# Kernel optimization log

Measured on AMD Instinct MI355X. Metric: run time of the kernel, lower is better.

## Reference

```python
import jax, jax.numpy as jnp
import numpy as np

B, N, HW, PS, FHW = 16, 4096, 224, 8, 56

def _gelu(x):
    return jax.nn.gelu(x, approximate=True)  # tanh approximation, matches nn.GELU(approximate='tanh')

def _conv(x, w, b, stride):
    y = jax.lax.conv_general_dilated(x, w, (stride, stride), [(1, 1), (1, 1)],
                                     dimension_numbers=('NCHW', 'OIHW', 'NCHW'))
    return y + b[None, :, None, None]

def _embed(points):
    # for i in 0..11: append sin(2^i * p) then cos(2^i * p) -> [B,N,48]
    factors = 2.0 ** jnp.arange(12, dtype=points.dtype)
    scaled = points[..., None, :] * factors[:, None]          # [B,N,12,2]
    feats = jnp.concatenate([jnp.sin(scaled), jnp.cos(scaled)], axis=-1)  # [B,N,12,4]
    return feats.reshape(points.shape[0], points.shape[1], 48)

def _extract_patches(fmap, points):
    # fmap [B,C,H,W]; points in [0,1]; bilinear grid_sample, zeros padding, align_corners=True
    Bq, C, H, W = fmap.shape
    centers = points * 2.0 - 1.0
    step = 2.0 / (W - 1)
    half = (PS - 1) / 2.0
    offs = jnp.linspace(-half, half, PS, dtype=fmap.dtype) * step
    offx2d, offy2d = jnp.meshgrid(offs, offs, indexing='ij')   # [ps,ps]
    gx = centers[..., 0][..., None, None] + offx2d             # [B,N,ps,ps]
    gy = centers[..., 1][..., None, None] + offy2d
    # align_corners=True pixel coords
    ix = (gx + 1.0) * 0.5 * (W - 1)
    iy = (gy + 1.0) * 0.5 * (H - 1)
    x0f = jnp.floor(ix); y0f = jnp.floor(iy)
    x0 = x0f.astype(jnp.int32); y0 = y0f.astype(jnp.int32)
    x1 = x0 + 1; y1 = y0 + 1
    wx1 = ix - x0f; wx0 = 1.0 - wx1
    wy1 = iy - y0f; wy0 = 1.0 - wy1
    fflat = fmap.reshape(Bq, C, H * W)

    def corner(xi, yi, w):
        valid = ((xi >= 0) & (xi < W) & (yi >= 0) & (yi < H)).astype(fmap.dtype)
        idx = jnp.clip(yi, 0, H - 1) * W + jnp.clip(xi, 0, W - 1)   # [B,N,ps,ps]
        vals = jax.vmap(lambda f, i: f[:, i])(fflat, idx)           # [B,C,N,ps,ps]
        return vals * (w * valid)[:, None]

    out = (corner(x0, y0, wx0 * wy0) + corner(x1, y0, wx1 * wy0)
           + corner(x0, y1, wx0 * wy1) + corner(x1, y1, wx1 * wy1))  # [B,C,N,ps,ps]
    return out.transpose(0, 2, 1, 3, 4)                              # [B,N,C,ps,ps]

def setup_inputs():
    key = jax.random.key(0)
    ks = jax.random.split(key, 26)
    def w(k, shape):
        fan_in = int(np.prod(shape[1:]))
        return jax.random.normal(k, shape, jnp.float32) * (1.0 / np.sqrt(fan_in))
    inp = {
        'points': jax.random.uniform(ks[0], (B, N, 2), jnp.float32),
        'images': jax.random.normal(ks[1], (B, 3, HW, HW), jnp.float32),
        # plane encoder
        'pw1': w(ks[2], (16, 3, 3, 3)),  'pb1': jnp.zeros((16,), jnp.float32),
        'pw2': w(ks[3], (32, 16, 3, 3)), 'pb2': jnp.zeros((32,), jnp.float32),
        'pw3': w(ks[4], (4, 32, 3, 3)),  'pb3': jnp.zeros((4,), jnp.float32),
        # global encoder
        'gw1': w(ks[5], (4, 3, 3, 3)),   'gb1': jnp.zeros((4,), jnp.float32),
        'gw2': w(ks[6], (8, 4, 3, 3)),   'gb2': jnp.zeros((8,), jnp.float32),
        'gw3': w(ks[7], (16, 8, 3, 3)),  'gb3': jnp.zeros((16,), jnp.float32),
        'gw4': w(ks[8], (32, 16, 3, 3)), 'gb4': jnp.zeros((32,), jnp.float32),
        'gw5': w(ks[9], (64, 32, 3, 3)), 'gb5': jnp.zeros((64,), jnp.float32),
        # point encoder (torch Linear: [out,in])
        'lw1': w(ks[10], (256, 48)),  'lb1': jnp.zeros((256,), jnp.float32),
        'lw2': w(ks[11], (256, 256)), 'lb2': jnp.zeros((256,), jnp.float32),
        # head
        'hw1': w(ks[12], (512, 576)), 'hb1': jnp.zeros((512,), jnp.float32),
        'hw2': w(ks[13], (1, 512)),   'hb2': jnp.zeros((1,), jnp.float32),
    }
    return inp

def reference(points, images, pw1, pb1, pw2, pb2, pw3, pb3,
              gw1, gb1, gw2, gb2, gw3, gb3, gw4, gb4, gw5, gb5,
              lw1, lb1, lw2, lb2, hw1, hb1, hw2, hb2):
    # point branch
    pe = _embed(points)                                         # [B,N,48]
    pf = _gelu(pe @ lw1.T + lb1) @ lw2.T + lb2                  # [B,N,256]
    # plane encoder -> 4x56x56 fmap
    f = _gelu(_conv(images, pw1, pb1, 2))
    f = _gelu(_conv(f, pw2, pb2, 2))
    fmap = _gelu(_conv(f, pw3, pb3, 1))                         # [B,4,56,56]
    # global encoder -> [B,64]
    g = images
    for wg, bg in ((gw1, gb1), (gw2, gb2), (gw3, gb3), (gw4, gb4), (gw5, gb5)):
        g = _gelu(_conv(g, wg, bg, 2))
    gc = g.mean(axis=(2, 3))                                    # AvgPool2d(7)+Flatten -> [B,64]
    gc = jnp.broadcast_to(gc[:, None, :], (points.shape[0], points.shape[1], 64))
    # per-point bilinear patch gather
    patches = _extract_patches(fmap, points).reshape(points.shape[0], points.shape[1], -1)  # [B,N,256]
    fused = jnp.concatenate([pf, patches, gc], axis=-1)         # [B,N,576]
    logit = _gelu(fused @ hw1.T + hb1) @ hw2.T + hb2            # [B,N,1]
    return logit
```

## Files before the change

kernel.cpp:

```cpp
#include <hip/hip_runtime.h>
#include <math.h>

#define BB 16
#define NN 4096
#define M_TOT (BB*NN)
#define TBK 32
#define HBK 64

typedef __attribute__((ext_vector_type(8))) short s8v;
typedef __attribute__((ext_vector_type(4))) float f4v;

__device__ __forceinline__ float gelu_t(float x){
    float u = 1.5957691216057308f * x * (1.0f + 0.044715f*x*x);
    return x / (1.0f + __expf(-u));
}

__device__ __forceinline__ unsigned short f2bf(float f){
    unsigned int u = __float_as_uint(f);
    u += 0x7fffu + ((u >> 16) & 1u);
    return (unsigned short)(u >> 16);
}

#define GLL(src, dst) __builtin_amdgcn_global_load_lds( \
    (const __attribute__((address_space(1))) void*)(src), \
    (__attribute__((address_space(3))) void*)(dst), 16, 0, 0)

template<int CIN, int COUT, int STRIDE, int CHUNK>
__device__ __forceinline__ void conv_dev2(
    const float* __restrict__ in, const float* __restrict__ w,
    const float* __restrict__ bias, float* __restrict__ out,
    int Hin, int Win, int Hout, int Wout, int bx, int by, int b, float* tile)
{
    constexpr int IW = 15*STRIDE + 3;
    constexpr int IH = IW;
    constexpr int PITCH = IW + 1;
    int tid = threadIdx.x;
    int tx = tid & 15, ty = tid >> 4;
    int wo = bx*16 + tx;
    int ho = by*16 + ty;
    int win0 = bx*16*STRIDE - 1;
    int hin0 = by*16*STRIDE - 1;
    bool valid = (wo < Wout) && (ho < Hout);

    float acc[COUT];
    #pragma unroll
    for (int co = 0; co < COUT; ++co) acc[co] = bias[co];

    const float* ib = in + (size_t)(b*CIN)*Hin*Win;
    for (int ci0 = 0; ci0 < CIN; ci0 += CHUNK) {
        __syncthreads();
        for (int idx = tid; idx < CHUNK*IH*IW; idx += 256) {
            int c = idx / (IH*IW), rem = idx - c*(IH*IW);
            int r = rem / IW, cc = rem - r*IW;
            int hi = hin0 + r, wi = win0 + cc;
            float v = 0.f;
            if ((unsigned)hi < (unsigned)Hin && (unsigned)wi < (unsigned)Win)
                v = ib[(size_t)(ci0 + c)*Hin*Win + hi*Win + wi];
            tile[c*IH*PITCH + r*PITCH + cc] = v;
        }
        __syncthreads();
        for (int ci = 0; ci < CHUNK; ++ci) {
            float vv[9];
            const float* tb = tile + ci*IH*PITCH;
            #pragma unroll
            for (int kh = 0; kh < 3; ++kh)
                #pragma unroll
                for (int kw = 0; kw < 3; ++kw)
                    vv[kh*3+kw] = tb[(ty*STRIDE + kh)*PITCH + tx*STRIDE + kw];
            const float* wc = w + (ci0 + ci)*9;
            #pragma unroll
            for (int co = 0; co < COUT; ++co) {
                const float* wp = wc + co*CIN*9;
                #pragma unroll
                for (int k = 0; k < 9; ++k)
                    acc[co] = fmaf(vv[k], wp[k], acc[co]);
            }
        }
    }
    if (valid) {
        size_t obase = ((size_t)b*COUT)*Hout*Wout + (size_t)ho*Wout + wo;
        #pragma unroll
        for (int co = 0; co < COUT; ++co)
            out[obase + (size_t)co*Hout*Wout] = gelu_t(acc[co]);
    }
}

__global__ __launch_bounds__(256) void conv_dual_k(
    const float* __restrict__ in,
    const float* __restrict__ wA, const float* __restrict__ bA,
    const float* __restrict__ wB, const float* __restrict__ bB,
    float* __restrict__ outA, float* __restrict__ outB)
{
    __shared__ float tile[3*33*34];
    const int Hin = 224, Win = 224, Hout = 112, Wout = 112;
    int tid = threadIdx.x;
    int tx = tid & 15, ty = tid >> 4;
    int b = blockIdx.z;
    int wo = blockIdx.x*16 + tx;
    int ho = blockIdx.y*16 + ty;
    int win0 = blockIdx.x*32 - 1;
    int hin0 = blockIdx.y*32 - 1;

    const float* ib = in + (size_t)(b*3)*Hin*Win;
    for (int idx = tid; idx < 3*1089; idx += 256) {
        int c = idx / 1089, rem = idx - c*1089;
        int r = rem / 33, cc = rem - r*33;
        int hi = hin0 + r, wi = win0 + cc;
        float v = 0.f;
        if ((unsigned)hi < (unsigned)Hin && (unsigned)wi < (unsigned)Win)
            v = ib[(size_t)c*Hin*Win + hi*Win + wi];
        tile[c*33*34 + r*34 + cc] = v;
    }
    __syncthreads();

    float accA[16], accB[4];
    #pragma unroll
    for (int co = 0; co < 16; ++co) accA[co] = bA[co];
    #pragma unroll
    for (int co = 0; co < 4; ++co) accB[co] = bB[co];

    #pragma unroll
    for (int ci = 0; ci < 3; ++ci) {
        float vv[9];
        const float* tb = tile + ci*33*34;
        #pragma unroll
        for (int kh = 0; kh < 3; ++kh)
            #pragma unroll
            for (int kw = 0; kw < 3; ++kw)
                vv[kh*3+kw] = tb[(ty*2 + kh)*34 + tx*2 + kw];
        #pragma unroll
        for (int co = 0; co < 16; ++co) {
            const float* wp = wA + co*27 + ci*9;
            #pragma unroll
            for (int k = 0; k < 9; ++k) accA[co] = fmaf(vv[k], wp[k], accA[co]);
        }
        #pragma unroll
        for (int co = 0; co < 4; ++co) {
            const float* wp = wB + co*27 + ci*9;
            #pragma unroll
            for (int k = 0; k < 9; ++k) accB[co] = fmaf(vv[k], wp[k], accB[co]);
        }
    }
    size_t px = (size_t)ho*Wout + wo;
    #pragma unroll
    for (int co = 0; co < 16; ++co)
        outA[((size_t)(b*16 + co))*Hout*Wout + px] = gelu_t(accA[co]);
    #pragma unroll
    for (int co = 0; co < 4; ++co)
        outB[((size_t)(b*4 + co))*Hout*Wout + px] = gelu_t(accB[co]);
}

__global__ __launch_bounds__(256) void conv_pg2_k(
    const float* __restrict__ f1, const float* __restrict__ pw2, const float* __restrict__ pb2, float* __restrict__ f2,
    const float* __restrict__ g1, const float* __restrict__ gw2, const float* __restrict__ gb2, float* __restrict__ g2)
{
    __shared__ float tile[8*33*34];
    int z = blockIdx.z;
    if (z < 32) {
        int b = z >> 1, half = z & 1;
        conv_dev2<16,16,2,8>(f1 + (size_t)b*16*12544, pw2 + half*2304, pb2 + half*16,
                             f2 + ((size_t)(b*32 + half*16))*3136,
                             112,112, 56,56, blockIdx.x, blockIdx.y, 0, tile);
    } else {
        conv_dev2<4,8,2,4>(g1, gw2, gb2, g2, 112,112, 56,56, blockIdx.x, blockIdx.y, z-32, tile);
    }
}

__global__ __launch_bounds__(256) void conv_pg3_k(
    const float* __restrict__ f2, const float* __restrict__ pw3, const float* __restrict__ pb3, float4* __restrict__ fmap4,
    const float* __restrict__ g2, const float* __restrict__ gw3, const float* __restrict__ gb3, float* __restrict__ g3)
{
    __shared__ float tile[8*33*34];
    int z = blockIdx.z;
    if (z < 16) {
        int b = z;
        int idx = blockIdx.x*256 + threadIdx.x;
        if (idx >= 3136) return;
        int ho = idx / 56, wo = idx - ho*56;
        const float* ib = f2 + (size_t)b*32*3136;
        float acc[4];
        #pragma unroll
        for (int co = 0; co < 4; ++co) acc[co] = pb3[co];
        for (int ci = 0; ci < 32; ++ci) {
            const float* ic = ib + (size_t)ci*3136;
            #pragma unroll
            for (int kh = 0; kh < 3; ++kh) {
                int hi = ho - 1 + kh;
                if ((unsigned)hi >= 56u) continue;
                #pragma unroll
                for (int kw = 0; kw < 3; ++kw) {
                    int wi = wo - 1 + kw;
                    if ((unsigned)wi >= 56u) continue;
                    float v = ic[hi*56 + wi];
                    int wofs = ci*9 + kh*3 + kw;
                    #pragma unroll
                    for (int co = 0; co < 4; ++co)
                        acc[co] = fmaf(v, pw3[co*288 + wofs], acc[co]);
                }
            }
        }
        float4 o;
        o.x = gelu_t(acc[0]); o.y = gelu_t(acc[1]);
        o.z = gelu_t(acc[2]); o.w = gelu_t(acc[3]);
        fmap4[(size_t)b*3136 + idx] = o;
    } else {
        if (blockIdx.x >= 4) return;
        int bx = blockIdx.x & 1, by = blockIdx.x >> 1;
        conv_dev2<8,16,2,8>(g2, gw3, gb3, g3, 56,56, 28,28, bx, by, z-16, tile);
    }
}

__global__ __launch_bounds__(256) void g4_k(
    const float* __restrict__ g3, const float* __restrict__ w4,
    const float* __restrict__ b4, float* __restrict__ g4o)
{
    int idx = blockIdx.x*256 + threadIdx.x;
    int co = idx & 31;
    int t = idx >> 5;
    int b = t / 196, px = t - b*196;
    int ho = px / 14, wo = px - ho*14;
    const float* src = g3 + (size_t)b*16*784;
    const float* wp = w4 + co*144;
    float acc = b4[co];
    for (int ci = 0; ci < 16; ++ci) {
        #pragma unroll
        for (int kh = 0; kh < 3; ++kh) {
            int hi = ho*2 - 1 + kh;
            if ((unsigned)hi >= 28u) continue;
            #pragma unroll
            for (int kw = 0; kw < 3; ++kw) {
                int wi = wo*2 - 1 + kw;
                if ((unsigned)wi >= 28u) continue;
                acc = fmaf(src[ci*784 + hi*28 + wi], wp[ci*9 + kh*3 + kw], acc);
            }
        }
    }
    g4o[(size_t)b*6272 + px*32 + co] = gelu_t(acc);
}

__global__ __launch_bounds__(256) void g5_k(
    const float* __restrict__ g4o, const float* __restrict__ w5,
    const float* __restrict__ b5, float* __restrict__ gc)
{
    int idx = blockIdx.x*256 + threadIdx.x;
    int co = idx & 63;
    int t = idx >> 6;
    int b = t / 49, px = t - b*49;
    int ho = px / 7, wo = px - ho*7;
    const float* src = g4o + (size_t)b*6272;
    const float* wp = w5 + co*288;
    float acc = b5[co];
    for (int ci = 0; ci < 32; ++ci) {
        #pragma unroll
        for (int kh = 0; kh < 3; ++kh) {
            int hi = ho*2 - 1 + kh;
            if ((unsigned)hi >= 14u) continue;
            #pragma unroll
            for (int kw = 0; kw < 3; ++kw) {
                int wi = wo*2 - 1 + kw;
                if ((unsigned)wi >= 14u) continue;
                acc = fmaf(src[(hi*14 + wi)*32 + ci], wp[ci*9 + kh*3 + kw], acc);
            }
        }
    }
    atomicAdd(&gc[b*64 + co], gelu_t(acc) * (1.0f/49.0f));
}

__global__ __launch_bounds__(256) void hgc_k(
    const float* __restrict__ gc, const float* __restrict__ hw1,
    const float* __restrict__ hb1, float* __restrict__ hgc)
{
    int idx = blockIdx.x*256 + threadIdx.x;
    int b = idx >> 9, n = idx & 511;
    const float* g = gc + b*64;
    const float* w = hw1 + (size_t)n*576 + 512;
    float s = hb1[n];
    #pragma unroll
    for (int c = 0; c < 64; ++c) s = fmaf(g[c], w[c], s);
    hgc[idx] = s;
}

__global__ void cvtall_k(const float* __restrict__ lw1, const float* __restrict__ lw2,
                         const float* __restrict__ hw1, unsigned short* __restrict__ blw1,
                         unsigned short* __restrict__ blw2, unsigned short* __restrict__ bhw1,
                         float* __restrict__ out, const float* __restrict__ b2,
                         float* __restrict__ gc){
    int i = blockIdx.x*blockDim.x + threadIdx.x;
    if (i < M_TOT) out[i] = b2[0];
    if (i < 1024) gc[i] = 0.f;
    if (i < 256*64) {
        int r = i >> 6, c = i & 63;
        blw1[i] = (c < 48) ? f2bf(lw1[r*48 + c]) : 0;
        return;
    }
    int j = i - 256*64;
    if (j < 256*256) { blw2[j] = f2bf(lw2[j]); return; }
    j -= 256*256;
    if (j < 512*576) bhw1[j] = f2bf(hw1[j]);
}

__global__ __launch_bounds__(512) void mlp12_k(
    const float* __restrict__ points,
    const unsigned short* __restrict__ W1, const float* __restrict__ b1,
    const unsigned short* __restrict__ W2, const float* __restrict__ b2,
    unsigned short* __restrict__ C,
    const float4* __restrict__ fmap4)
{
    __shared__ unsigned short Hd[128*256];
    int tid = threadIdx.x;
    int wv = tid >> 6, lane = tid & 63;
    int q = lane >> 4, lr = lane & 15;
    int mi = wv >> 2, ni = wv & 3;
    size_t m0 = (size_t)blockIdx.x * 128;

    f4v acc1[4][4];
    #pragma unroll
    for (int i = 0; i < 4; ++i)
        #pragma unroll
        for (int j = 0; j < 4; ++j) acc1[i][j] = (f4v){0.f,0.f,0.f,0.f};

    #pragma unroll
    for (int kb = 0; kb < 2; ++kb) {
        int seg = kb*4 + q;
        s8v a[4], b[4];
        #pragma unroll
        for (int t = 0; t < 4; ++t) {
            size_t m = m0 + mi*64 + t*16 + lr;
            float px = points[m*2], py = points[m*2+1];
            union { s8v v; unsigned short u[8]; } pk;
            #pragma unroll
            for (int j = 0; j < 8; ++j) {
                int k = seg*8 + j;
                unsigned short val = 0;
                if (k < 48) {
                    int i2 = k >> 2, rr = k & 3;
                    float f = (float)(1 << i2);
                    float p = (rr & 1) ? py : px;
                    float s = f * p;
                    val = f2bf((rr < 2) ? __sinf(s) : __cosf(s));
                }
                pk.u[j] = val;
            }
            a[t] = pk.v;
        }
        #pragma unroll
        for (int t = 0; t < 4; ++t) {
            int n = ni*64 + t*16 + lr;
            b[t] = *(const s8v*)(W1 + n*64 + seg*8);
        }
        #pragma unroll
        for (int mt = 0; mt < 4; ++mt)
            #pragma unroll
            for (int nt = 0; nt < 4; ++nt)
                acc1[mt][nt] = __builtin_amdgcn_mfma_f32_16x16x32_bf16(a[mt], b[nt], acc1[mt][nt], 0, 0, 0);
    }
    {
        float b1v[4];
        #pragma unroll
        for (int nt = 0; nt < 4; ++nt) b1v[nt] = b1[ni*64 + nt*16 + lr];
        #pragma unroll
        for (int mt = 0; mt < 4; ++mt)
            #pragma unroll
            for (int r4 = 0; r4 < 4; ++r4) {
                int row = mi*64 + mt*16 + q*4 + r4;
                #pragma unroll
                for (int nt = 0; nt < 4; ++nt) {
                    int col = ni*64 + nt*16 + lr;
                    float v = gelu_t(acc1[mt][nt][r4] + b1v[nt]);
                    int p = (col >> 3) ^ (row & 7);
                    Hd[(row*32 + p)*8 + (col & 7)] = f2bf(v);
                }
            }
    }
    __syncthreads();

    f4v acc2[4][4];
    #pragma unroll
    for (int i = 0; i < 4; ++i)
        #pragma unroll
        for (int j = 0; j < 4; ++j) acc2[i][j] = (f4v){0.f,0.f,0.f,0.f};

    #pragma unroll 2
    for (int kt = 0; kt < 8; ++kt) {
        s8v a[4], b[4];
        #pragma unroll
        for (int t = 0; t < 4; ++t) {
            int n = ni*64 + t*16 + lr;
            b[t] = *(const s8v*)(W2 + (size_t)n*256 + kt*32 + q*8);
        }
        #pragma unroll
        for (int t = 0; t < 4; ++t) {
            int row = mi*64 + t*16 + lr;
            int p = (kt*4 + q) ^ (row & 7);
            a[t] = *(const s8v*)(Hd + (row*32 + p)*8);
        }
        #pragma unroll
        for (int mt = 0; mt < 4; ++mt)
            #pragma unroll
            for (int nt = 0; nt < 4; ++nt)
                acc2[mt][nt] = __builtin_amdgcn_mfma_f32_16x16x32_bf16(a[mt], b[nt], acc2[mt][nt], 0, 0, 0);
    }
    {
        float b2v[4];
        #pragma unroll
        for (int nt = 0; nt < 4; ++nt) b2v[nt] = b2[ni*64 + nt*16 + lr];
        #pragma unroll
        for (int mt = 0; mt < 4; ++mt)
            #pragma unroll
            for (int r4 = 0; r4 < 4; ++r4) {
                size_t m = m0 + mi*64 + mt*16 + q*4 + r4;
                #pragma unroll
                for (int nt = 0; nt < 4; ++nt) {
                    int n = ni*64 + nt*16 + lr;
                    C[m*512 + n] = f2bf(acc2[mt][nt][r4] + b2v[nt]);
                }
            }
    }
    #pragma unroll 2
    for (int it = 0; it < 16; ++it) {
        int task = it*512 + tid;
        int ml = task >> 6, ij = task & 63;
        size_t m = m0 + ml;
        int i = ij >> 3, j = ij & 7;
        int b = (int)(m >> 12);
        float px = points[m*2], py = points[m*2+1];
        float cx = px*2.f - 1.f, cy = py*2.f - 1.f;
        const float step = 2.0f/55.0f;
        float gx = cx + ((float)i - 3.5f)*step;
        float gy = cy + ((float)j - 3.5f)*step;
        float ix = (gx + 1.f)*0.5f*55.f;
        float iy = (gy + 1.f)*0.5f*55.f;
        float x0f = floorf(ix), y0f = floorf(iy);
        int x0 = (int)x0f, y0 = (int)y0f;
        int x1 = x0 + 1,  y1 = y0 + 1;
        float wx1 = ix - x0f, wx0 = 1.f - wx1;
        float wy1 = iy - y0f, wy0 = 1.f - wy1;
        float v00 = ((x0>=0)&&(x0<56)&&(y0>=0)&&(y0<56)) ? 1.f : 0.f;
        float v10 = ((x1>=0)&&(x1<56)&&(y0>=0)&&(y0<56)) ? 1.f : 0.f;
        float v01 = ((x0>=0)&&(x0<56)&&(y1>=0)&&(y1<56)) ? 1.f : 0.f;
        float v11 = ((x1>=0)&&(x1<56)&&(y1>=0)&&(y1<56)) ? 1.f : 0.f;
        float w00 = wx0*wy0*v00, w10 = wx1*wy0*v10, w01 = wx0*wy1*v01, w11 = wx1*wy1*v11;
        int cx0 = min(max(x0,0),55), cx1 = min(max(x1,0),55);
        int cy0 = min(max(y0,0),55), cy1 = min(max(y1,0),55);
        const float4* fb = fmap4 + (size_t)b*3136;
        float4 f00 = fb[cy0*56 + cx0], f10 = fb[cy0*56 + cx1];
        float4 f01 = fb[cy1*56 + cx0], f11 = fb[cy1*56 + cx1];
        float4 v;
        v.x = w00*f00.x + w10*f10.x + w01*f01.x + w11*f11.x;
        v.y = w00*f00.y + w10*f10.y + w01*f01.y + w11*f11.y;
        v.z = w00*f00.z + w10*f10.z + w01*f01.z + w11*f11.z;
        v.w = w00*f00.w + w10*f10.w + w01*f01.w + w11*f11.w;
        C[m*512 + 256 +   0 + ij] = f2bf(v.x);
        C[m*512 + 256 +  64 + ij] = f2bf(v.y);
        C[m*512 + 256 + 128 + ij] = f2bf(v.z);
        C[m*512 + 256 + 192 + ij] = f2bf(v.w);
    }
}

__global__ __launch_bounds__(256, 3) void gemm_hd_k(
    const unsigned short* __restrict__ A,
    const unsigned short* __restrict__ W,
    const float* __restrict__ hgc, const float* __restrict__ w2,
    float* __restrict__ out)
{
    __shared__ unsigned short As[64*HBK];
    __shared__ unsigned short Bs[256*HBK];
    __shared__ float red[4*64];
    int tid = threadIdx.x;
    int wv = tid >> 6, lane = tid & 63;
    int q = lane >> 4, lr = lane & 15;
    int nq = wv * 64;
    size_t m0 = (size_t)blockIdx.x * 64;
    int nbase = blockIdx.y * 256;
    int bimg = (int)(m0 >> 12);

    const unsigned short* srcA[2]; unsigned short* dstA[2];
    #pragma unroll
    for (int r = 0; r < 2; ++r) {
        int f = r*256 + tid;
        int row = f >> 3, sl = (f & 7) ^ (row & 7);
        srcA[r] = A + (m0 + row)*512 + sl*8;
        dstA[r] = As + f*8;
    }
    const unsigned short* srcB[8]; unsigned short* dstB[8];
    #pragma unroll
    for (int r = 0; r < 8; ++r) {
        int f = r*256 + tid;
        int row = f >> 3, sl = (f & 7) ^ (row & 7);
        srcB[r] = W + (size_t)(nbase + row)*576 + sl*8;
        dstB[r] = Bs + f*8;
    }

    f4v acc[4][4];
    #pragma unroll
    for (int i = 0; i < 4; ++i)
        #pragma unroll
        for (int j = 0; j < 4; ++j) acc[i][j] = (f4v){0.f,0.f,0.f,0.f};

    for (int k0 = 0; k0 < 512; k0 += HBK) {
        #pragma unroll
        for (int r = 0; r < 2; ++r) { GLL(srcA[r], dstA[r]); srcA[r] += HBK; }
        #pragma unroll
        for (int r = 0; r < 8; ++r) { GLL(srcB[r], dstB[r]); srcB[r] += HBK; }
        __syncthreads();
        #pragma unroll
        for (int kk = 0; kk < 2; ++kk) {
            s8v a[4], b[4];
            #pragma unroll
            for (int t = 0; t < 4; ++t) {
                int row = t*16 + lr;
                int ph = (kk*4 + q) ^ (row & 7);
                a[t] = *(const s8v*)(As + (row*8 + ph)*8);
            }
            #pragma unroll
            for (int t = 0; t < 4; ++t) {
                int row = nq + t*16 + lr;
                int ph = (kk*4 + q) ^ (row & 7);
                b[t] = *(const s8v*)(Bs + (row*8 + ph)*8);
            }
            #pragma unroll
            for (int mt = 0; mt < 4; ++mt)
                #pragma unroll
                for (int nt = 0; nt < 4; ++nt)
                    acc[mt][nt] = __builtin_amdgcn_mfma_f32_16x16x32_bf16(a[mt], b[nt], acc[mt][nt], 0, 0, 0);
        }
        __syncthreads();
    }
    float bv[4], w2v[4];
    #pragma unroll
    for (int nt = 0; nt < 4; ++nt) {
        int n = nbase + nq + nt*16 + lr;
        bv[nt] = hgc[bimg*512 + n];
        w2v[nt] = w2[n];
    }
    #pragma unroll
    for (int mt = 0; mt < 4; ++mt)
        #pragma unroll
        for (int r4 = 0; r4 < 4; ++r4) {
            int ml = mt*16 + q*4 + r4;
            float s = 0.f;
            #pragma unroll
            for (int nt = 0; nt < 4; ++nt)
                s += gelu_t(acc[mt][nt][r4] + bv[nt]) * w2v[nt];
            #pragma unroll
            for (int off = 8; off > 0; off >>= 1) s += __shfl_down(s, off, 16);
            if (lr == 0) red[wv*64 + ml] = s;
        }
    __syncthreads();
    if (tid < 64) {
        float t = red[tid] + red[64 + tid] + red[128 + tid] + red[192 + tid];
        atomicAdd(&out[m0 + tid], t);
    }
}

extern "C" void kernel_launch(void* const* d_in, const int* in_sizes, int n_in,
                              void* d_out, int out_size, void* d_ws, size_t ws_size,
                              hipStream_t stream) {
    const float* points = (const float*)d_in[0];
    const float* images = (const float*)d_in[1];
    const float* pw1 = (const float*)d_in[2];  const float* pb1 = (const float*)d_in[3];
    const float* pw2 = (const float*)d_in[4];  const float* pb2 = (const float*)d_in[5];
    const float* pw3 = (const float*)d_in[6];  const float* pb3 = (const float*)d_in[7];
    const float* gw1 = (const float*)d_in[8];  const float* gb1 = (const float*)d_in[9];
    const float* gw2 = (const float*)d_in[10]; const float* gb2 = (const float*)d_in[11];
    const float* gw3 = (const float*)d_in[12]; const float* gb3 = (const float*)d_in[13];
    const float* gw4 = (const float*)d_in[14]; const float* gb4 = (const float*)d_in[15];
    const float* gw5 = (const float*)d_in[16]; const float* gb5 = (const float*)d_in[17];
    const float* lw1 = (const float*)d_in[18]; const float* lb1 = (const float*)d_in[19];
    const float* lw2 = (const float*)d_in[20]; const float* lb2 = (const float*)d_in[21];
    const float* hw1 = (const float*)d_in[22]; const float* hb1 = (const float*)d_in[23];
    const float* hw2 = (const float*)d_in[24]; const float* hb2 = (const float*)d_in[25];
    float* out = (float*)d_out;

    char* base = (char*)d_ws;
    unsigned short* fused_b = (unsigned short*)base;
    float4* fmap4 = (float4*)(fused_b + (size_t)M_TOT*512);
    float* gc   = (float*)(fmap4 + (size_t)16*3136);
    float* hgc  = gc + 1024;
    unsigned short* blw1 = (unsigned short*)(hgc + 16*512);
    unsigned short* blw2 = blw1 + 256*64;
    unsigned short* bhw1 = blw2 + 256*256;
    float* ct = (float*)base;
    float* f1 = ct;
    float* f2 = f1 + (size_t)16*16*112*112;
    float* g1 = f2 + (size_t)16*32*56*56;
    float* g2 = g1 + (size_t)16*4*112*112;
    float* g3 = g2 + (size_t)16*8*56*56;
    float* g4 = g3 + (size_t)16*16*28*28;

    cvtall_k<<<1472, 256, 0, stream>>>(lw1, lw2, hw1, blw1, blw2, bhw1, out, hb2, gc);
    conv_dual_k<<<dim3(7,7,16), 256, 0, stream>>>(images, pw1, pb1, gw1, gb1, f1, g1);
    conv_pg2_k<<<dim3(4,4,48), 256, 0, stream>>>(f1, pw2, pb2, f2, g1, gw2, gb2, g2);
    conv_pg3_k<<<dim3(13,1,32), 256, 0, stream>>>(f2, pw3, pb3, fmap4, g2, gw3, gb3, g3);
    g4_k<<<392, 256, 0, stream>>>(g3, gw4, gb4, g4);
    g5_k<<<196, 256, 0, stream>>>(g4, gw5, gb5, gc);
    hgc_k<<<32, 256, 0, stream>>>(gc, hw1, hb1, hgc);
    mlp12_k<<<M_TOT/128, 512, 0, stream>>>(points, blw1, lb1, blw2, lb2, fused_b, fmap4);
    gemm_hd_k<<<dim3(M_TOT/64, 2), 256, 0, stream>>>(fused_b, bhw1, hgc, hw2, out);
}
```

Baseline: 427.7 us.

## Move patch gather into g4 kernel, stage positional embedding in LDS, permute hw1 columns

The bilinear patch gather leaves the point-MLP kernel and runs as extra blocks of the small g4 conv launch, so the tiny conv4 work shares one launch with the gather. The gather now writes four channels at a time as one ushort4 store, and the matching hw1 columns are permuted during bf16 conversion so the head GEMM still sees the right order. The MLP kernel computes the sin/cos embedding once per element into swizzled LDS instead of redundantly per wave. g3 and g4o move out of the aliased conv scratch region, because that region overlaps the fused buffer that the gather now writes before the convs' outputs are consumed.

```diff
diff --git a/kernel.cpp b/kernel.cpp
--- a/kernel.cpp
+++ b/kernel.cpp
@@ -4,7 +4,6 @@
 #define BB 16
 #define NN 4096
 #define M_TOT (BB*NN)
-#define TBK 32
 #define HBK 64
 
 typedef __attribute__((ext_vector_type(8))) short s8v;
@@ -210,217 +209,41 @@
     }
 }
 
-__global__ __launch_bounds__(256) void g4_k(
+__global__ __launch_bounds__(256) void k4_k(
     const float* __restrict__ g3, const float* __restrict__ w4,
-    const float* __restrict__ b4, float* __restrict__ g4o)
-{
-    int idx = blockIdx.x*256 + threadIdx.x;
-    int co = idx & 31;
-    int t = idx >> 5;
-    int b = t / 196, px = t - b*196;
-    int ho = px / 14, wo = px - ho*14;
-    const float* src = g3 + (size_t)b*16*784;
-    const float* wp = w4 + co*144;
-    float acc = b4[co];
-    for (int ci = 0; ci < 16; ++ci) {
-        #pragma unroll
-        for (int kh = 0; kh < 3; ++kh) {
-            int hi = ho*2 - 1 + kh;
-            if ((unsigned)hi >= 28u) continue;
-            #pragma unroll
-            for (int kw = 0; kw < 3; ++kw) {
-                int wi = wo*2 - 1 + kw;
-                if ((unsigned)wi >= 28u) continue;
-                acc = fmaf(src[ci*784 + hi*28 + wi], wp[ci*9 + kh*3 + kw], acc);
-            }
-        }
-    }
-    g4o[(size_t)b*6272 + px*32 + co] = gelu_t(acc);
-}
-
-__global__ __launch_bounds__(256) void g5_k(
-    const float* __restrict__ g4o, const float* __restrict__ w5,
-    const float* __restrict__ b5, float* __restrict__ gc)
-{
-    int idx = blockIdx.x*256 + threadIdx.x;
-    int co = idx & 63;
-    int t = idx >> 6;
-    int b = t / 49, px = t - b*49;
-    int ho = px / 7, wo = px - ho*7;
-    const float* src = g4o + (size_t)b*6272;
-    const float* wp = w5 + co*288;
-    float acc = b5[co];
-    for (int ci = 0; ci < 32; ++ci) {
-        #pragma unroll
-        for (int kh = 0; kh < 3; ++kh) {
-            int hi = ho*2 - 1 + kh;
-            if ((unsigned)hi >= 14u) continue;
-            #pragma unroll
-            for (int kw = 0; kw < 3; ++kw) {
-                int wi = wo*2 - 1 + kw;
-                if ((unsigned)wi >= 14u) continue;
-                acc = fmaf(src[(hi*14 + wi)*32 + ci], wp[ci*9 + kh*3 + kw], acc);
-            }
-        }
-    }
-    atomicAdd(&gc[b*64 + co], gelu_t(acc) * (1.0f/49.0f));
-}
-
-__global__ __launch_bounds__(256) void hgc_k(
-    const float* __restrict__ gc, const float* __restrict__ hw1,
-    const float* __restrict__ hb1, float* __restrict__ hgc)
-{
-    int idx = blockIdx.x*256 + threadIdx.x;
-    int b = idx >> 9, n = idx & 511;
-    const float* g = gc + b*64;
-    const float* w = hw1 + (size_t)n*576 + 512;
-    float s = hb1[n];
-    #pragma unroll
-    for (int c = 0; c < 64; ++c) s = fmaf(g[c], w[c], s);
-    hgc[idx] = s;
-}
-
-__global__ void cvtall_k(const float* __restrict__ lw1, const float* __restrict__ lw2,
-                         const float* __restrict__ hw1, unsigned short* __restrict__ blw1,
-                         unsigned short* __restrict__ blw2, unsigned short* __restrict__ bhw1,
-                         float* __restrict__ out, const float* __restrict__ b2,
-                         float* __restrict__ gc){
-    int i = blockIdx.x*blockDim.x + threadIdx.x;
-    if (i < M_TOT) out[i] = b2[0];
-    if (i < 1024) gc[i] = 0.f;
-    if (i < 256*64) {
-        int r = i >> 6, c = i & 63;
-        blw1[i] = (c < 48) ? f2bf(lw1[r*48 + c]) : 0;
-        return;
-    }
-    int j = i - 256*64;
-    if (j < 256*256) { blw2[j] = f2bf(lw2[j]); return; }
-    j -= 256*256;
-    if (j < 512*576) bhw1[j] = f2bf(hw1[j]);
-}
-
-__global__ __launch_bounds__(512) void mlp12_k(
-    const float* __restrict__ points,
-    const unsigned short* __restrict__ W1, const float* __restrict__ b1,
-    const unsigned short* __restrict__ W2, const float* __restrict__ b2,
-    unsigned short* __restrict__ C,
-    const float4* __restrict__ fmap4)
-{
-    __shared__ unsigned short Hd[128*256];
+    const float* __restrict__ b4, float* __restrict__ g4o,
+    const float4* __restrict__ fmap4, const float* __restrict__ points,
+    unsigned short* __restrict__ C)
+{
+    int bid = blockIdx.x;
     int tid = threadIdx.x;
-    int wv = tid >> 6, lane = tid & 63;
-    int q = lane >> 4, lr = lane & 15;
-    int mi = wv >> 2, ni = wv & 3;
-    size_t m0 = (size_t)blockIdx.x * 128;
-
-    f4v acc1[4][4];
-    #pragma unroll
-    for (int i = 0; i < 4; ++i)
-        #pragma unroll
-        for (int j = 0; j < 4; ++j) acc1[i][j] = (f4v){0.f,0.f,0.f,0.f};
-
-    #pragma unroll
-    for (int kb = 0; kb < 2; ++kb) {
-        int seg = kb*4 + q;
-        s8v a[4], b[4];
-        #pragma unroll
-        for (int t = 0; t < 4; ++t) {
-            size_t m = m0 + mi*64 + t*16 + lr;
-            float px = points[m*2], py = points[m*2+1];
-            union { s8v v; unsigned short u[8]; } pk;
-            #pragma unroll
-            for (int j = 0; j < 8; ++j) {
-                int k = seg*8 + j;
-                unsigned short val = 0;
-                if (k < 48) {
-                    int i2 = k >> 2, rr = k & 3;
-                    float f = (float)(1 << i2);
-                    float p = (rr & 1) ? py : px;
-                    float s = f * p;
-                    val = f2bf((rr < 2) ? __sinf(s) : __cosf(s));
+    if (bid < 392) {
+        int idx = bid*256 + tid;
+        int co = idx & 31;
+        int t = idx >> 5;
+        int b = t / 196, px = t - b*196;
+        int ho = px / 14, wo = px - ho*14;
+        const float* src = g3 + (size_t)b*16*784;
+        const float* wp = w4 + co*144;
+        float acc = b4[co];
+        for (int ci = 0; ci < 16; ++ci) {
+            #pragma unroll
+            for (int kh = 0; kh < 3; ++kh) {
+                int hi = ho*2 - 1 + kh;
+                if ((unsigned)hi >= 28u) continue;
+                #pragma unroll
+                for (int kw = 0; kw < 3; ++kw) {
+                    int wi = wo*2 - 1 + kw;
+                    if ((unsigned)wi >= 28u) continue;
+                    acc = fmaf(src[ci*784 + hi*28 + wi], wp[ci*9 + kh*3 + kw], acc);
                 }
-                pk.u[j] = val;
-            }
-            a[t] = pk.v;
-        }
-        #pragma unroll
-        for (int t = 0; t < 4; ++t) {
-            int n = ni*64 + t*16 + lr;
-            b[t] = *(const s8v*)(W1 + n*64 + seg*8);
-        }
-        #pragma unroll
-        for (int mt = 0; mt < 4; ++mt)
-            #pragma unroll
-            for (int nt = 0; nt < 4; ++nt)
-                acc1[mt][nt] = __builtin_amdgcn_mfma_f32_16x16x32_bf16(a[mt], b[nt], acc1[mt][nt], 0, 0, 0);
-    }
-    {
-        float b1v[4];
-        #pragma unroll
-        for (int nt = 0; nt < 4; ++nt) b1v[nt] = b1[ni*64 + nt*16 + lr];
-        #pragma unroll
-        for (int mt = 0; mt < 4; ++mt)
-            #pragma unroll
-            for (int r4 = 0; r4 < 4; ++r4) {
-                int row = mi*64 + mt*16 + q*4 + r4;
-                #pragma unroll
-                for (int nt = 0; nt < 4; ++nt) {
-                    int col = ni*64 + nt*16 + lr;
-                    float v = gelu_t(acc1[mt][nt][r4] + b1v[nt]);
-                    int p = (col >> 3) ^ (row & 7);
-                    Hd[(row*32 + p)*8 + (col & 7)] = f2bf(v);
-                }
-            }
-    }
-    __syncthreads();
-
-    f4v acc2[4][4];
-    #pragma unroll
-    for (int i = 0; i < 4; ++i)
-        #pragma unroll
-        for (int j = 0; j < 4; ++j) acc2[i][j] = (f4v){0.f,0.f,0.f,0.f};
-
-    #pragma unroll 2
-    for (int kt = 0; kt < 8; ++kt) {
-        s8v a[4], b[4];
-        #pragma unroll
-        for (int t = 0; t < 4; ++t) {
-            int n = ni*64 + t*16 + lr;
-            b[t] = *(const s8v*)(W2 + (size_t)n*256 + kt*32 + q*8);
-        }
-        #pragma unroll
-        for (int t = 0; t < 4; ++t) {
-            int row = mi*64 + t*16 + lr;
-            int p = (kt*4 + q) ^ (row & 7);
-            a[t] = *(const s8v*)(Hd + (row*32 + p)*8);
-        }
-        #pragma unroll
-        for (int mt = 0; mt < 4; ++mt)
-            #pragma unroll
-            for (int nt = 0; nt < 4; ++nt)
-                acc2[mt][nt] = __builtin_amdgcn_mfma_f32_16x16x32_bf16(a[mt], b[nt], acc2[mt][nt], 0, 0, 0);
-    }
-    {
-        float b2v[4];
-        #pragma unroll
-        for (int nt = 0; nt < 4; ++nt) b2v[nt] = b2[ni*64 + nt*16 + lr];
-        #pragma unroll
-        for (int mt = 0; mt < 4; ++mt)
-            #pragma unroll
-            for (int r4 = 0; r4 < 4; ++r4) {
-                size_t m = m0 + mi*64 + mt*16 + q*4 + r4;
-                #pragma unroll
-                for (int nt = 0; nt < 4; ++nt) {
-                    int n = ni*64 + nt*16 + lr;
-                    C[m*512 + n] = f2bf(acc2[mt][nt][r4] + b2v[nt]);
-                }
-            }
-    }
-    #pragma unroll 2
-    for (int it = 0; it < 16; ++it) {
-        int task = it*512 + tid;
+            }
+        }
+        g4o[(size_t)b*6272 + px*32 + co] = gelu_t(acc);
+    } else {
+        int task = (bid - 392)*256 + tid;
         int ml = task >> 6, ij = task & 63;
-        size_t m = m0 + ml;
+        size_t m = (size_t)ml;
         int i = ij >> 3, j = ij & 7;
         int b = (int)(m >> 12);
         float px = points[m*2], py = points[m*2+1];
@@ -450,10 +273,206 @@
         v.y = w00*f00.y + w10*f10.y + w01*f01.y + w11*f11.y;
         v.z = w00*f00.z + w10*f10.z + w01*f01.z + w11*f11.z;
         v.w = w00*f00.w + w10*f10.w + w01*f01.w + w11*f11.w;
-        C[m*512 + 256 +   0 + ij] = f2bf(v.x);
-        C[m*512 + 256 +  64 + ij] = f2bf(v.y);
-        C[m*512 + 256 + 128 + ij] = f2bf(v.z);
-        C[m*512 + 256 + 192 + ij] = f2bf(v.w);
+        ushort4 o;
+        o.x = f2bf(v.x); o.y = f2bf(v.y); o.z = f2bf(v.z); o.w = f2bf(v.w);
+        *(ushort4*)(C + m*512 + 256 + ij*4) = o;
+    }
+}
+
+__global__ __launch_bounds__(256) void g5_k(
+    const float* __restrict__ g4o, const float* __restrict__ w5,
+    const float* __restrict__ b5, float* __restrict__ gc)
+{
+    int idx = blockIdx.x*256 + threadIdx.x;
+    int co = idx & 63;
+    int t = idx >> 6;
+    int b = t / 49, px = t - b*49;
+    int ho = px / 7, wo = px - ho*7;
+    const float* src = g4o + (size_t)b*6272;
+    const float* wp = w5 + co*288;
+    float acc = b5[co];
+    for (int ci = 0; ci < 32; ++ci) {
+        #pragma unroll
+        for (int kh = 0; kh < 3; ++kh) {
+            int hi = ho*2 - 1 + kh;
+            if ((unsigned)hi >= 14u) continue;
+            #pragma unroll
+            for (int kw = 0; kw < 3; ++kw) {
+                int wi = wo*2 - 1 + kw;
+                if ((unsigned)wi >= 14u) continue;
+                acc = fmaf(src[(hi*14 + wi)*32 + ci], wp[ci*9 + kh*3 + kw], acc);
+            }
+        }
+    }
+    atomicAdd(&gc[b*64 + co], gelu_t(acc) * (1.0f/49.0f));
+}
+
+__global__ __launch_bounds__(256) void hgc_k(
+    const float* __restrict__ gc, const float* __restrict__ hw1,
+    const float* __restrict__ hb1, float* __restrict__ hgc)
+{
+    int idx = blockIdx.x*256 + threadIdx.x;
+    int b = idx >> 9, n = idx & 511;
+    const float* g = gc + b*64;
+    const float* w = hw1 + (size_t)n*576 + 512;
+    float s = hb1[n];
+    #pragma unroll
+    for (int c = 0; c < 64; ++c) s = fmaf(g[c], w[c], s);
+    hgc[idx] = s;
+}
+
+__global__ void cvtall_k(const float* __restrict__ lw1, const float* __restrict__ lw2,
+                         const float* __restrict__ hw1, unsigned short* __restrict__ blw1,
+                         unsigned short* __restrict__ blw2, unsigned short* __restrict__ bhw1,
+                         float* __restrict__ out, const float* __restrict__ b2,
+                         float* __restrict__ gc){
+    int i = blockIdx.x*blockDim.x + threadIdx.x;
+    if (i < M_TOT) out[i] = b2[0];
+    if (i < 1024) gc[i] = 0.f;
+    if (i < 256*64) {
+        int r = i >> 6, c = i & 63;
+        blw1[i] = (c < 48) ? f2bf(lw1[r*48 + c]) : 0;
+        return;
+    }
+    int j = i - 256*64;
+    if (j < 256*256) { blw2[j] = f2bf(lw2[j]); return; }
+    j -= 256*256;
+    if (j < 512*576) {
+        int n = j / 576, k = j - n*576;
+        int src_k = k;
+        if (k >= 256 && k < 512) {
+            int s = k - 256;
+            src_k = 256 + (s & 3)*64 + (s >> 2);
+        }
+        bhw1[j] = f2bf(hw1[(size_t)n*576 + src_k]);
+    }
+}
+
+__global__ __launch_bounds__(512) void mlp12_k(
+    const float* __restrict__ points,
+    const unsigned short* __restrict__ W1, const float* __restrict__ b1,
+    const unsigned short* __restrict__ W2, const float* __restrict__ b2,
+    unsigned short* __restrict__ C)
+{
+    __shared__ unsigned short Pe[128*64];
+    __shared__ unsigned short Hd[128*256];
+    int tid = threadIdx.x;
+    int wv = tid >> 6, lane = tid & 63;
+    int q = lane >> 4, lr = lane & 15;
+    int mi = wv >> 2, ni = wv & 3;
+    size_t m0 = (size_t)blockIdx.x * 128;
+
+    #pragma unroll
+    for (int it = 0; it < 2; ++it) {
+        int idx = it*512 + tid;
+        int row = idx >> 3, seg = idx & 7;
+        size_t m = m0 + row;
+        float px = points[m*2], py = points[m*2+1];
+        union { s8v v; unsigned short u[8]; } pk;
+        #pragma unroll
+        for (int j = 0; j < 8; ++j) {
+            int k = seg*8 + j;
+            unsigned short val = 0;
+            if (k < 48) {
+                int i2 = k >> 2, rr = k & 3;
+                float f = (float)(1 << i2);
+                float p = (rr & 1) ? py : px;
+                float s = f * p;
+                val = f2bf((rr < 2) ? __sinf(s) : __cosf(s));
+            }
+            pk.u[j] = val;
+        }
+        *(s8v*)(Pe + (row*8 + (seg ^ (row & 7)))*8) = pk.v;
+    }
+    __syncthreads();
+
+    f4v acc1[4][4];
+    #pragma unroll
+    for (int i = 0; i < 4; ++i)
+        #pragma unroll
+        for (int j = 0; j < 4; ++j) acc1[i][j] = (f4v){0.f,0.f,0.f,0.f};
+
+    #pragma unroll
+    for (int kb = 0; kb < 2; ++kb) {
+        int seg = kb*4 + q;
+        s8v a[4], b[4];
+        #pragma unroll
+        for (int t = 0; t < 4; ++t) {
+            int row = mi*64 + t*16 + lr;
+            a[t] = *(const s8v*)(Pe + (row*8 + (seg ^ (row & 7)))*8);
+        }
+        #pragma unroll
+        for (int t = 0; t < 4; ++t) {
+            int n = ni*64 + t*16 + lr;
+            b[t] = *(const s8v*)(W1 + n*64 + seg*8);
+        }
+        #pragma unroll
+        for (int mt = 0; mt < 4; ++mt)
+            #pragma unroll
+            for (int nt = 0; nt < 4; ++nt)
+                acc1[mt][nt] = __builtin_amdgcn_mfma_f32_16x16x32_bf16(a[mt], b[nt], acc1[mt][nt], 0, 0, 0);
+    }
+    {
+        float b1v[4];
+        #pragma unroll
+        for (int nt = 0; nt < 4; ++nt) b1v[nt] = b1[ni*64 + nt*16 + lr];
+        #pragma unroll
+        for (int mt = 0; mt < 4; ++mt)
+            #pragma unroll
+            for (int r4 = 0; r4 < 4; ++r4) {
+                int row = mi*64 + mt*16 + q*4 + r4;
+                #pragma unroll
+                for (int nt = 0; nt < 4; ++nt) {
+                    int col = ni*64 + nt*16 + lr;
+                    float v = gelu_t(acc1[mt][nt][r4] + b1v[nt]);
+                    int p = (col >> 3) ^ (row & 7);
+                    Hd[(row*32 + p)*8 + (col & 7)] = f2bf(v);
+                }
+            }
+    }
+    __syncthreads();
+
+    f4v acc2[4][4];
+    #pragma unroll
+    for (int i = 0; i < 4; ++i)
+        #pragma unroll
+        for (int j = 0; j < 4; ++j) acc2[i][j] = (f4v){0.f,0.f,0.f,0.f};
+
+    #pragma unroll 2
+    for (int kt = 0; kt < 8; ++kt) {
+        s8v a[4], b[4];
+        #pragma unroll
+        for (int t = 0; t < 4; ++t) {
+            int n = ni*64 + t*16 + lr;
+            b[t] = *(const s8v*)(W2 + (size_t)n*256 + kt*32 + q*8);
+        }
+        #pragma unroll
+        for (int t = 0; t < 4; ++t) {
+            int row = mi*64 + t*16 + lr;
+            int p = (kt*4 + q) ^ (row & 7);
+            a[t] = *(const s8v*)(Hd + (row*32 + p)*8);
+        }
+        #pragma unroll
+        for (int mt = 0; mt < 4; ++mt)
+            #pragma unroll
+            for (int nt = 0; nt < 4; ++nt)
+                acc2[mt][nt] = __builtin_amdgcn_mfma_f32_16x16x32_bf16(a[mt], b[nt], acc2[mt][nt], 0, 0, 0);
+    }
+    {
+        float b2v[4];
+        #pragma unroll
+        for (int nt = 0; nt < 4; ++nt) b2v[nt] = b2[ni*64 + nt*16 + lr];
+        #pragma unroll
+        for (int mt = 0; mt < 4; ++mt)
+            #pragma unroll
+            for (int r4 = 0; r4 < 4; ++r4) {
+                size_t m = m0 + mi*64 + mt*16 + q*4 + r4;
+                #pragma unroll
+                for (int nt = 0; nt < 4; ++nt) {
+                    int n = ni*64 + nt*16 + lr;
+                    C[m*512 + n] = f2bf(acc2[mt][nt][r4] + b2v[nt]);
+                }
+            }
     }
 }
 
@@ -575,7 +594,9 @@
     char* base = (char*)d_ws;
     unsigned short* fused_b = (unsigned short*)base;
     float4* fmap4 = (float4*)(fused_b + (size_t)M_TOT*512);
-    float* gc   = (float*)(fmap4 + (size_t)16*3136);
+    float* g3   = (float*)(fmap4 + (size_t)16*3136);
+    float* g4o  = g3 + (size_t)16*16*784;
+    float* gc   = g4o + (size_t)16*32*196;
     float* hgc  = gc + 1024;
     unsigned short* blw1 = (unsigned short*)(hgc + 16*512);
     unsigned short* blw2 = blw1 + 256*64;
@@ -585,16 +606,14 @@
     float* f2 = f1 + (size_t)16*16*112*112;
     float* g1 = f2 + (size_t)16*32*56*56;
     float* g2 = g1 + (size_t)16*4*112*112;
-    float* g3 = g2 + (size_t)16*8*56*56;
-    float* g4 = g3 + (size_t)16*16*28*28;
 
     cvtall_k<<<1472, 256, 0, stream>>>(lw1, lw2, hw1, blw1, blw2, bhw1, out, hb2, gc);
     conv_dual_k<<<dim3(7,7,16), 256, 0, stream>>>(images, pw1, pb1, gw1, gb1, f1, g1);
     conv_pg2_k<<<dim3(4,4,48), 256, 0, stream>>>(f1, pw2, pb2, f2, g1, gw2, gb2, g2);
     conv_pg3_k<<<dim3(13,1,32), 256, 0, stream>>>(f2, pw3, pb3, fmap4, g2, gw3, gb3, g3);
-    g4_k<<<392, 256, 0, stream>>>(g3, gw4, gb4, g4);
-    g5_k<<<196, 256, 0, stream>>>(g4, gw5, gb5, gc);
+    k4_k<<<392 + 16384, 256, 0, stream>>>(g3, gw4, gb4, g4o, fmap4, points, fused_b);
+    g5_k<<<196, 256, 0, stream>>>(g4o, gw5, gb5, gc);
     hgc_k<<<32, 256, 0, stream>>>(gc, hw1, hb1, hgc);
-    mlp12_k<<<M_TOT/128, 512, 0, stream>>>(points, blw1, lb1, blw2, lb2, fused_b, fmap4);
+    mlp12_k<<<M_TOT/128, 512, 0, stream>>>(points, blw1, lb1, blw2, lb2, fused_b);
     gemm_hd_k<<<dim3(M_TOT/64, 2), 256, 0, stream>>>(fused_b, bhw1, hgc, hw2, out);
 }
```

New measurement: 419.4 us. Within noise of the previous version (-1.9%).
